# Kernel tuning notes

Measured on AMD Instinct MI355X. Metric: run time of the kernel, lower is better.

## Reference

```python
import jax, jax.numpy as jnp
import numpy as np

# Layered type graph: L layers of M nodes; layer 0 = basic types, layers >=1 reference earlier layers only.
L, M, D, P, S = 64, 2048, 128, 4, 2
NB = 11  # number of Kotlin basic types (kotlin.Any ... kotlin.Unit)
N = L * M


def setup_inputs() -> dict:
    key = jax.random.key(0)
    ks = jax.random.split(key, 8)
    rng = np.random.default_rng(0)
    basic_names = jnp.asarray(rng.integers(0, NB, size=(M,)), dtype=jnp.int32)
    # properties / superTypes point strictly to earlier layers (valid topological DAG)
    prop_ids = np.zeros((L, M, P), dtype=np.int32)
    super_ids = np.zeros((L, M, S), dtype=np.int32)
    for l in range(1, L):
        prop_ids[l] = rng.integers(0, l * M, size=(M, P))
        super_ids[l] = rng.integers(0, l * M, size=(M, S))
    prop_ids = jnp.asarray(prop_ids)
    super_ids = jnp.asarray(super_ids)
    sc = 0.05
    return {
        "basic_names": basic_names,
        "prop_ids": prop_ids,
        "super_ids": super_ids,
        "basic_table": jax.random.normal(ks[0], (NB, D), jnp.float32) * sc,
        "W_m": jax.random.normal(ks[1], (D, 4 * D), jnp.float32) * sc,
        "U_m": jax.random.normal(ks[2], (D, 4 * D), jnp.float32) * sc,
        "b_m": jnp.zeros((4 * D,), jnp.float32),
        "W_s": jax.random.normal(ks[3], (D, 4 * D), jnp.float32) * sc,
        "U_s": jax.random.normal(ks[4], (D, 4 * D), jnp.float32) * sc,
        "b_s": jnp.zeros((4 * D,), jnp.float32),
        "empty_members": jax.random.normal(ks[5], (D,), jnp.float32) * sc,
    }


def _lstm_last(seq, W, U, b):
    # seq: [T, B, D]; keras LSTM (tanh / sigmoid, gate order i,f,g,o); returns last hidden [B, D]
    T, B, Dh = seq.shape
    h = jnp.zeros((B, Dh), seq.dtype)
    c = jnp.zeros((B, Dh), seq.dtype)
    for t in range(T):  # T is a small static constant (P+1 or S+1)
        z = seq[t] @ W + h @ U + b  # [B, 4D]
        i, f, g, o = jnp.split(z, 4, axis=-1)
        c = jax.nn.sigmoid(f) * c + jax.nn.sigmoid(i) * jnp.tanh(g)
        h = jax.nn.sigmoid(o) * jnp.tanh(c)
    return h


def reference(basic_names, prop_ids, super_ids, basic_table, W_m, U_m, b_m, W_s, U_s, b_s, empty_members):
    emb = jnp.zeros((N, D), basic_table.dtype)
    emb = emb.at[:M].set(basic_table[basic_names])  # layer 0: basic type embedding lookup

    def step(emb, xs):
        l, pid, sid = xs  # pid:[M,P] sid:[M,S], all indices < l*M (already computed)
        prop_e = jnp.swapaxes(emb[pid], 0, 1)  # [P, M, D] irregular gather
        seq_m = jnp.concatenate([jnp.broadcast_to(empty_members, (1, M, D)), prop_e], axis=0)  # [P+1, M, D]
        h_m = _lstm_last(seq_m, W_m, U_m, b_m)  # embed_members
        sup_e = jnp.swapaxes(emb[sid], 0, 1)  # [S, M, D]
        seq_s = jnp.concatenate([sup_e, h_m[None]], axis=0)  # [S+1, M, D]
        h_s = _lstm_last(seq_s, W_s, U_s, b_s)  # embed_super_types
        emb = jax.lax.dynamic_update_slice(emb, h_s, (l * M, 0))
        return emb, None

    ls = jnp.arange(1, L, dtype=jnp.int32)
    emb, _ = jax.lax.scan(step, emb, (ls, prop_ids[1:], super_ids[1:]))
    return emb  # [N, D] == tf.convert_to_tensor(class_embeddings)
```

## Files before the change

kernel.cpp:

```cpp
#include <hip/hip_runtime.h>

typedef unsigned short u16;
typedef short s16x8 __attribute__((ext_vector_type(8)));
typedef float f32x4 __attribute__((ext_vector_type(4)));

#define LAYERS   64
#define M_NODES  2048
#define DIM      128
#define FD       512
#define CHUNK    16
#define NBLK     128
#define TPB      512
#define XPAD     136

__device__ __forceinline__ u16 f2bf(float f) {
    union { float f; unsigned int i; } v; v.f = f;
    unsigned int r = (v.i + 0x7FFFu + ((v.i >> 16) & 1u)) >> 16;
    return (u16)r;
}
__device__ __forceinline__ float sigm(float x) {
    return __builtin_amdgcn_rcpf(1.0f + __builtin_exp2f(-1.44269504f * x));
}
__device__ __forceinline__ float tanh_f(float x) {
    float ax = __builtin_fabsf(x);
    float t  = __builtin_exp2f(-2.88539008f * ax);
    float r  = (1.0f - t) * __builtin_amdgcn_rcpf(1.0f + t);
    return __builtin_copysignf(r, x);
}

__global__ void l0_kernel(const int* __restrict__ names, const float* __restrict__ table,
                          float* __restrict__ emb) {
    int v = blockIdx.x * blockDim.x + threadIdx.x;
    if (v >= M_NODES * (DIM / 4)) return;
    int row = v >> 5, c = v & 31;
    const float4* src = (const float4*)(table + (size_t)names[row] * DIM);
    ((float4*)(emb + (size_t)row * DIM))[c] = src[c];
}

__global__ void repack_kernel(const float* __restrict__ Wm, const float* __restrict__ Um,
                              const float* __restrict__ Ws, const float* __restrict__ Us,
                              u16* __restrict__ packed) {
    int t = blockIdx.x * blockDim.x + threadIdx.x;
    if (t >= 4 * 4 * 32 * 64) return;
    int lane = t & 63, ntg = (t >> 6) & 31, kc = (t >> 11) & 3, mat = t >> 13;
    const float* B = (mat == 0) ? Wm : (mat == 1) ? Um : (mat == 2) ? Ws : Us;
    int q = lane >> 4, nl = lane & 15;
    int kb = kc * 32 + q * 8;
    int n  = ntg * 16 + nl;
    u16* dst = packed + ((((size_t)mat * 4 + kc) * 32 + ntg) * 64 + lane) * 8;
    #pragma unroll
    for (int j = 0; j < 8; j++) dst[j] = f2bf(B[(size_t)(kb + j) * FD + n]);
}

template <bool PACKED>
__global__ __launch_bounds__(TPB, 2) void layer_kernel(
    float* __restrict__ emb, const int* __restrict__ prop_ids, const int* __restrict__ super_ids,
    const float* __restrict__ Wm, const float* __restrict__ Um, const float* __restrict__ bm,
    const float* __restrict__ Ws, const float* __restrict__ Us, const float* __restrict__ bs,
    const float* __restrict__ empty, const u16* __restrict__ packed, int l) {

    __shared__ __align__(16) u16  xs[6][CHUNK][XPAD];
    __shared__ __align__(16) u16  hbuf[2][CHUNK][XPAD];
    __shared__ __align__(16) u16  empty_s[XPAD];

    const int tid  = threadIdx.x;
    const int b    = blockIdx.x;
    const int g0   = b * CHUNK;
    const size_t row0 = (size_t)l * M_NODES + g0;

    const int wv   = tid >> 6;
    const int lane = tid & 63;
    const int q    = lane >> 4, nl = lane & 15;
    const int d    = wv * 16 + nl;

    if (tid < 384) {
        int quarter = tid & 3;
        int r    = tid >> 2;
        int slot = r >> 4;
        int node = r & 15;
        size_t idx;
        if (slot < 4) idx = (size_t)prop_ids [((size_t)l * M_NODES + g0 + node) * 4 + slot];
        else          idx = (size_t)super_ids[((size_t)l * M_NODES + g0 + node) * 2 + (slot - 4)];
        const float4* src = (const float4*)(emb + idx * DIM);
        u16* dst = &xs[slot][node][0];
        int e0 = quarter * 32;
        #pragma unroll
        for (int j = 0; j < 8; j++) {
            float4 v = src[(e0 >> 2) + j];
            int o = e0 + j * 4;
            dst[o] = f2bf(v.x); dst[o + 1] = f2bf(v.y);
            dst[o + 2] = f2bf(v.z); dst[o + 3] = f2bf(v.w);
        }
    } else if (tid < 384 + 128) {
        int dd = tid - 384;
        empty_s[dd] = f2bf(empty[dd]);
    }
    __syncthreads();

    auto load_bfrag_packed = [&](int mat, int kc, int g) -> s16x8 {
        return *(const s16x8*)(packed + ((((size_t)mat * 4 + kc) * 32 + (g * 8 + wv)) * 64 + lane) * 8);
    };
    auto load_bfrag_direct = [&](const float* B, int kc, int g) -> s16x8 {
        int kb = kc * 32 + q * 8;
        int n  = g * 128 + d;
        s16x8 f;
        #pragma unroll
        for (int j = 0; j < 8; j++) f[j] = (short)f2bf(B[(size_t)(kb + j) * FD + n]);
        return f;
    };
    auto load_afrag = [&](const u16* X , int kc) -> s16x8 {
        return *(const s16x8*)(X + (size_t)nl * XPAD + kc * 32 + q * 8);
    };

    auto run_phase = [&](const float* Wg, const float* Ug, const float* bias,
                         int matW, int matU, int nsteps, const int* slots,
                         bool write_hm, bool write_out) {
        s16x8 wf[4][4], uf[4][4];
        #pragma unroll
        for (int kc = 0; kc < 4; kc++) {
            #pragma unroll
            for (int g = 0; g < 4; g++) {
                if (PACKED) { wf[kc][g] = load_bfrag_packed(matW, kc, g);
                              uf[kc][g] = load_bfrag_packed(matU, kc, g); }
                else        { wf[kc][g] = load_bfrag_direct(Wg, kc, g);
                              uf[kc][g] = load_bfrag_direct(Ug, kc, g); }
            }
        }
        float bz[4];
        #pragma unroll
        for (int g = 0; g < 4; g++) bz[g] = bias[g * 128 + d];
        float cc[4] = {0.f, 0.f, 0.f, 0.f};

        #pragma unroll 1
        for (int t = 0; t < nsteps; t++) {
            int s = slots[t];
            f32x4 acc[4];
            #pragma unroll
            for (int g = 0; g < 4; g++) acc[g] = (f32x4){0.f, 0.f, 0.f, 0.f};
            #pragma unroll
            for (int kc = 0; kc < 4; kc++) {
                s16x8 a = (s < 0) ? *(const s16x8*)(&empty_s[kc * 32 + q * 8])
                                  : load_afrag(&xs[s][0][0], kc);
                #pragma unroll
                for (int g = 0; g < 4; g++)
                    acc[g] = __builtin_amdgcn_mfma_f32_16x16x32_bf16(a, wf[kc][g], acc[g], 0, 0, 0);
            }
            if (t > 0) {
                __syncthreads();
                const u16* hb = &hbuf[(t - 1) & 1][0][0];
                #pragma unroll
                for (int kc = 0; kc < 4; kc++) {
                    s16x8 a = load_afrag(hb, kc);
                    #pragma unroll
                    for (int g = 0; g < 4; g++)
                        acc[g] = __builtin_amdgcn_mfma_f32_16x16x32_bf16(a, uf[kc][g], acc[g], 0, 0, 0);
                }
            }
            bool last = (t == nsteps - 1);
            #pragma unroll
            for (int r2 = 0; r2 < 4; r2++) {
                int m = q * 4 + r2;
                float zi = acc[0][r2] + bz[0];
                float zf = acc[1][r2] + bz[1];
                float zg = acc[2][r2] + bz[2];
                float zo = acc[3][r2] + bz[3];
                float c  = sigm(zf) * cc[r2] + sigm(zi) * tanh_f(zg);
                cc[r2] = c;
                float h  = sigm(zo) * tanh_f(c);
                if (!last)          hbuf[t & 1][m][d] = f2bf(h);
                else if (write_hm)  xs[0][m][d] = f2bf(h);
                else if (write_out) emb[(row0 + m) * DIM + d] = h;
            }
        }
    };

    {
        const int slots_m[5] = {-1, 0, 1, 2, 3};
        run_phase(Wm, Um, bm, 0, 1, 5, slots_m, true, false);
    }
    {
        const int slots_s[3] = {4, 5, 0};
        run_phase(Ws, Us, bs, 2, 3, 3, slots_s, false, true);
    }
}

extern "C" void kernel_launch(void* const* d_in, const int* in_sizes, int n_in,
                              void* d_out, int out_size, void* d_ws, size_t ws_size,
                              hipStream_t stream) {
    const int*   names = (const int*)d_in[0];
    const int*   pids  = (const int*)d_in[1];
    const int*   sids  = (const int*)d_in[2];
    const float* table = (const float*)d_in[3];
    const float* Wm    = (const float*)d_in[4];
    const float* Um    = (const float*)d_in[5];
    const float* bm    = (const float*)d_in[6];
    const float* Ws    = (const float*)d_in[7];
    const float* Us    = (const float*)d_in[8];
    const float* bs    = (const float*)d_in[9];
    const float* empt  = (const float*)d_in[10];
    float* emb  = (float*)d_out;
    u16* packed = (u16*)d_ws;

    l0_kernel<<<256, 256, 0, stream>>>(names, table, emb);

    const size_t packed_bytes = (size_t)4 * 4 * 32 * 64 * 8 * sizeof(u16);
    if (ws_size >= packed_bytes) {
        repack_kernel<<<128, 256, 0, stream>>>(Wm, Um, Ws, Us, packed);
        for (int l = 1; l < LAYERS; l++)
            layer_kernel<true><<<NBLK, TPB, 0, stream>>>(emb, pids, sids, Wm, Um, bm,
                                                         Ws, Us, bs, empt, packed, l);
    } else {
        for (int l = 1; l < LAYERS; l++)
            layer_kernel<false><<<NBLK, TPB, 0, stream>>>(emb, pids, sids, Wm, Um, bm,
                                                          Ws, Us, bs, empt, packed, l);
    }
}
```

Baseline: 1.269 ms.

## Replace per-layer launches with persistent cooperative kernel and global atomic barrier

```diff
diff --git a/kernel.cpp b/kernel.cpp
--- a/kernel.cpp
+++ b/kernel.cpp
@@ -52,85 +52,176 @@
     for (int j = 0; j < 8; j++) dst[j] = f2bf(B[(size_t)(kb + j) * FD + n]);
 }
 
-template <bool PACKED>
-__global__ __launch_bounds__(TPB, 2) void layer_kernel(
+__global__ void init_bar(int* bar) { if (threadIdx.x < 2) bar[threadIdx.x] = 0; }
+
+__device__ __forceinline__ s16x8 load_bfrag(const u16* __restrict__ packed,
+                                            int mat, int kc, int ntile, int lane) {
+    return *(const s16x8*)(packed + ((((size_t)mat * 4 + kc) * 32 + ntile) * 64 + lane) * 8);
+}
+
+template<int NSTEPS>
+__device__ __forceinline__ void lstm_phase(
+    const u16* __restrict__ packed, const int matW, const int matU,
+    const float* __restrict__ bz , const int* slots,
+    u16 (*xs)[CHUNK][XPAD], u16 (*hbuf)[CHUNK][XPAD], const u16* empty_s,
+    float* __restrict__ out ,
+    const int wv, const int lane)
+{
+    const int q = lane >> 4, nl = lane & 15;
+    const int d = wv * 16 + nl;
+    s16x8 wf[4][4], uf[4][4];
+    #pragma unroll
+    for (int kc = 0; kc < 4; kc++)
+        #pragma unroll
+        for (int g = 0; g < 4; g++) {
+            wf[kc][g] = load_bfrag(packed, matW, kc, g * 8 + wv, lane);
+            uf[kc][g] = load_bfrag(packed, matU, kc, g * 8 + wv, lane);
+        }
+    float cc[4] = {0.f, 0.f, 0.f, 0.f};
+    #pragma unroll
+    for (int t = 0; t < NSTEPS; t++) {
+        const int s = slots[t];
+        f32x4 acc[4];
+        #pragma unroll
+        for (int g = 0; g < 4; g++) acc[g] = (f32x4){0.f, 0.f, 0.f, 0.f};
+        #pragma unroll
+        for (int kc = 0; kc < 4; kc++) {
+            s16x8 a = (s < 0) ? *(const s16x8*)(empty_s + kc * 32 + q * 8)
+                              : *(const s16x8*)(&xs[s][nl][kc * 32 + q * 8]);
+            #pragma unroll
+            for (int g = 0; g < 4; g++)
+                acc[g] = __builtin_amdgcn_mfma_f32_16x16x32_bf16(a, wf[kc][g], acc[g], 0, 0, 0);
+        }
+        if (t > 0) {
+            __syncthreads();
+            #pragma unroll
+            for (int kc = 0; kc < 4; kc++) {
+                s16x8 a = *(const s16x8*)(&hbuf[(t - 1) & 1][nl][kc * 32 + q * 8]);
+                #pragma unroll
+                for (int g = 0; g < 4; g++)
+                    acc[g] = __builtin_amdgcn_mfma_f32_16x16x32_bf16(a, uf[kc][g], acc[g], 0, 0, 0);
+            }
+        }
+        const bool last = (t == NSTEPS - 1);
+        #pragma unroll
+        for (int r2 = 0; r2 < 4; r2++) {
+            int m = q * 4 + r2;
+            float zi = acc[0][r2] + bz[0];
+            float zf = acc[1][r2] + bz[1];
+            float zg = acc[2][r2] + bz[2];
+            float zo = acc[3][r2] + bz[3];
+            float c  = sigm(zf) * cc[r2] + sigm(zi) * tanh_f(zg);
+            cc[r2] = c;
+            float h  = sigm(zo) * tanh_f(c);
+            if (!last)            hbuf[t & 1][m][d] = f2bf(h);
+            else if (out == nullptr) xs[0][m][d] = f2bf(h);
+            else                  out[(size_t)m * DIM + d] = h;
+        }
+    }
+}
+
+__global__ __launch_bounds__(TPB, 2) void persist_kernel(
+    float* __restrict__ emb, const int* __restrict__ prop_ids, const int* __restrict__ super_ids,
+    const float* __restrict__ bm, const float* __restrict__ bs,
+    const float* __restrict__ empty, const u16* __restrict__ packed, int* bar) {
+
+    __shared__ __align__(16) u16  xs[6][CHUNK][XPAD];
+    __shared__ __align__(16) u16  hbuf[2][CHUNK][XPAD];
+    __shared__ __align__(16) u16  empty_s[XPAD];
+
+    const int tid  = threadIdx.x;
+    const int g0   = blockIdx.x * CHUNK;
+    const int wv   = tid >> 6;
+    const int lane = tid & 63;
+    const int d    = wv * 16 + (lane & 15);
+
+    if (tid < DIM) empty_s[tid] = f2bf(empty[tid]);
+    float bzm[4], bzs[4];
+    #pragma unroll
+    for (int g = 0; g < 4; g++) { bzm[g] = bm[g * 128 + d]; bzs[g] = bs[g * 128 + d]; }
+
+    const int c32  = tid & 31;
+    const int node = tid >> 5;
+
+    #pragma unroll 1
+    for (int l = 1; l < LAYERS; l++) {
+        #pragma unroll
+        for (int k = 0; k < 6; k++) {
+            int idx = (k < 4) ? prop_ids [((size_t)l * M_NODES + g0 + node) * 4 + k]
+                              : super_ids[((size_t)l * M_NODES + g0 + node) * 2 + (k - 4)];
+            float4 v = ((const float4*)(emb + (size_t)idx * DIM))[c32];
+            u16* dst = &xs[k][node][c32 * 4];
+            dst[0] = f2bf(v.x); dst[1] = f2bf(v.y); dst[2] = f2bf(v.z); dst[3] = f2bf(v.w);
+        }
+        __syncthreads();
+
+        const int slots_m[5] = {-1, 0, 1, 2, 3};
+        lstm_phase<5>(packed, 0, 1, bzm, slots_m, xs, hbuf, empty_s, nullptr, wv, lane);
+        const int slots_s[3] = {4, 5, 0};
+        lstm_phase<3>(packed, 2, 3, bzs, slots_s, xs, hbuf, empty_s,
+                      emb + ((size_t)l * M_NODES + g0) * DIM, wv, lane);
+
+        if (l < LAYERS - 1) {
+            __syncthreads();
+            if (tid == 0) {
+                __builtin_amdgcn_fence(__ATOMIC_RELEASE, "agent");
+                __hip_atomic_fetch_add(bar, 1, __ATOMIC_RELAXED, __HIP_MEMORY_SCOPE_AGENT);
+                const int target = l * NBLK;
+                while (__hip_atomic_load(bar, __ATOMIC_RELAXED, __HIP_MEMORY_SCOPE_AGENT) < target)
+                    __builtin_amdgcn_s_sleep(2);
+                __builtin_amdgcn_fence(__ATOMIC_ACQUIRE, "agent");
+            }
+            __syncthreads();
+        }
+    }
+}
+
+__global__ __launch_bounds__(TPB, 2) void layer_fallback(
     float* __restrict__ emb, const int* __restrict__ prop_ids, const int* __restrict__ super_ids,
     const float* __restrict__ Wm, const float* __restrict__ Um, const float* __restrict__ bm,
     const float* __restrict__ Ws, const float* __restrict__ Us, const float* __restrict__ bs,
-    const float* __restrict__ empty, const u16* __restrict__ packed, int l) {
+    const float* __restrict__ empty, int l) {
 
     __shared__ __align__(16) u16  xs[6][CHUNK][XPAD];
     __shared__ __align__(16) u16  hbuf[2][CHUNK][XPAD];
     __shared__ __align__(16) u16  empty_s[XPAD];
 
     const int tid  = threadIdx.x;
-    const int b    = blockIdx.x;
-    const int g0   = b * CHUNK;
-    const size_t row0 = (size_t)l * M_NODES + g0;
-
-    const int wv   = tid >> 6;
-    const int lane = tid & 63;
+    const int g0   = blockIdx.x * CHUNK;
+    const int wv   = tid >> 6, lane = tid & 63;
     const int q    = lane >> 4, nl = lane & 15;
     const int d    = wv * 16 + nl;
-
-    if (tid < 384) {
-        int quarter = tid & 3;
-        int r    = tid >> 2;
-        int slot = r >> 4;
-        int node = r & 15;
-        size_t idx;
-        if (slot < 4) idx = (size_t)prop_ids [((size_t)l * M_NODES + g0 + node) * 4 + slot];
-        else          idx = (size_t)super_ids[((size_t)l * M_NODES + g0 + node) * 2 + (slot - 4)];
-        const float4* src = (const float4*)(emb + idx * DIM);
-        u16* dst = &xs[slot][node][0];
-        int e0 = quarter * 32;
-        #pragma unroll
-        for (int j = 0; j < 8; j++) {
-            float4 v = src[(e0 >> 2) + j];
-            int o = e0 + j * 4;
-            dst[o] = f2bf(v.x); dst[o + 1] = f2bf(v.y);
-            dst[o + 2] = f2bf(v.z); dst[o + 3] = f2bf(v.w);
-        }
-    } else if (tid < 384 + 128) {
-        int dd = tid - 384;
-        empty_s[dd] = f2bf(empty[dd]);
+    const int c32  = tid & 31, node = tid >> 5;
+
+    if (tid < DIM) empty_s[tid] = f2bf(empty[tid]);
+    #pragma unroll
+    for (int k = 0; k < 6; k++) {
+        int idx = (k < 4) ? prop_ids [((size_t)l * M_NODES + g0 + node) * 4 + k]
+                          : super_ids[((size_t)l * M_NODES + g0 + node) * 2 + (k - 4)];
+        float4 v = ((const float4*)(emb + (size_t)idx * DIM))[c32];
+        u16* dst = &xs[k][node][c32 * 4];
+        dst[0] = f2bf(v.x); dst[1] = f2bf(v.y); dst[2] = f2bf(v.z); dst[3] = f2bf(v.w);
     }
     __syncthreads();
 
-    auto load_bfrag_packed = [&](int mat, int kc, int g) -> s16x8 {
-        return *(const s16x8*)(packed + ((((size_t)mat * 4 + kc) * 32 + (g * 8 + wv)) * 64 + lane) * 8);
-    };
-    auto load_bfrag_direct = [&](const float* B, int kc, int g) -> s16x8 {
-        int kb = kc * 32 + q * 8;
-        int n  = g * 128 + d;
+    auto direct = [&](const float* B, int kc, int g) -> s16x8 {
+        int kb = kc * 32 + q * 8, n = g * 128 + d;
         s16x8 f;
         #pragma unroll
         for (int j = 0; j < 8; j++) f[j] = (short)f2bf(B[(size_t)(kb + j) * FD + n]);
         return f;
     };
-    auto load_afrag = [&](const u16* X , int kc) -> s16x8 {
-        return *(const s16x8*)(X + (size_t)nl * XPAD + kc * 32 + q * 8);
-    };
-
-    auto run_phase = [&](const float* Wg, const float* Ug, const float* bias,
-                         int matW, int matU, int nsteps, const int* slots,
-                         bool write_hm, bool write_out) {
+    auto run = [&](const float* W, const float* U, const float* bias,
+                   int nsteps, const int* slots, float* out) {
         s16x8 wf[4][4], uf[4][4];
         #pragma unroll
-        for (int kc = 0; kc < 4; kc++) {
-            #pragma unroll
-            for (int g = 0; g < 4; g++) {
-                if (PACKED) { wf[kc][g] = load_bfrag_packed(matW, kc, g);
-                              uf[kc][g] = load_bfrag_packed(matU, kc, g); }
-                else        { wf[kc][g] = load_bfrag_direct(Wg, kc, g);
-                              uf[kc][g] = load_bfrag_direct(Ug, kc, g); }
-            }
-        }
+        for (int kc = 0; kc < 4; kc++)
+            #pragma unroll
+            for (int g = 0; g < 4; g++) { wf[kc][g] = direct(W, kc, g); uf[kc][g] = direct(U, kc, g); }
         float bz[4];
         #pragma unroll
         for (int g = 0; g < 4; g++) bz[g] = bias[g * 128 + d];
         float cc[4] = {0.f, 0.f, 0.f, 0.f};
-
         #pragma unroll 1
         for (int t = 0; t < nsteps; t++) {
             int s = slots[t];
@@ -139,18 +230,17 @@
             for (int g = 0; g < 4; g++) acc[g] = (f32x4){0.f, 0.f, 0.f, 0.f};
             #pragma unroll
             for (int kc = 0; kc < 4; kc++) {
-                s16x8 a = (s < 0) ? *(const s16x8*)(&empty_s[kc * 32 + q * 8])
-                                  : load_afrag(&xs[s][0][0], kc);
+                s16x8 a = (s < 0) ? *(const s16x8*)(empty_s + kc * 32 + q * 8)
+                                  : *(const s16x8*)(&xs[s][nl][kc * 32 + q * 8]);
                 #pragma unroll
                 for (int g = 0; g < 4; g++)
                     acc[g] = __builtin_amdgcn_mfma_f32_16x16x32_bf16(a, wf[kc][g], acc[g], 0, 0, 0);
             }
             if (t > 0) {
                 __syncthreads();
-                const u16* hb = &hbuf[(t - 1) & 1][0][0];
                 #pragma unroll
                 for (int kc = 0; kc < 4; kc++) {
-                    s16x8 a = load_afrag(hb, kc);
+                    s16x8 a = *(const s16x8*)(&hbuf[(t - 1) & 1][nl][kc * 32 + q * 8]);
                     #pragma unroll
                     for (int g = 0; g < 4; g++)
                         acc[g] = __builtin_amdgcn_mfma_f32_16x16x32_bf16(a, uf[kc][g], acc[g], 0, 0, 0);
@@ -167,21 +257,16 @@
                 float c  = sigm(zf) * cc[r2] + sigm(zi) * tanh_f(zg);
                 cc[r2] = c;
                 float h  = sigm(zo) * tanh_f(c);
-                if (!last)          hbuf[t & 1][m][d] = f2bf(h);
-                else if (write_hm)  xs[0][m][d] = f2bf(h);
-                else if (write_out) emb[(row0 + m) * DIM + d] = h;
+                if (!last)               hbuf[t & 1][m][d] = f2bf(h);
+                else if (out == nullptr) xs[0][m][d] = f2bf(h);
+                else                     out[(size_t)m * DIM + d] = h;
             }
         }
     };
-
-    {
-        const int slots_m[5] = {-1, 0, 1, 2, 3};
-        run_phase(Wm, Um, bm, 0, 1, 5, slots_m, true, false);
-    }
-    {
-        const int slots_s[3] = {4, 5, 0};
-        run_phase(Ws, Us, bs, 2, 3, 3, slots_s, false, true);
-    }
+    const int slots_m[5] = {-1, 0, 1, 2, 3};
+    run(Wm, Um, bm, 5, slots_m, nullptr);
+    const int slots_s[3] = {4, 5, 0};
+    run(Ws, Us, bs, 3, slots_s, emb + ((size_t)l * M_NODES + g0) * DIM);
 }
 
 extern "C" void kernel_launch(void* const* d_in, const int* in_sizes, int n_in,
@@ -199,19 +284,23 @@
     const float* bs    = (const float*)d_in[9];
     const float* empt  = (const float*)d_in[10];
     float* emb  = (float*)d_out;
+
+    const size_t packed_bytes = (size_t)4 * 4 * 32 * 64 * 8 * sizeof(u16);
     u16* packed = (u16*)d_ws;
+    int* bar    = (int*)((char*)d_ws + packed_bytes);
 
     l0_kernel<<<256, 256, 0, stream>>>(names, table, emb);
 
-    const size_t packed_bytes = (size_t)4 * 4 * 32 * 64 * 8 * sizeof(u16);
-    if (ws_size >= packed_bytes) {
+    if (ws_size >= packed_bytes + 256) {
         repack_kernel<<<128, 256, 0, stream>>>(Wm, Um, Ws, Us, packed);
-        for (int l = 1; l < LAYERS; l++)
-            layer_kernel<true><<<NBLK, TPB, 0, stream>>>(emb, pids, sids, Wm, Um, bm,
-                                                         Ws, Us, bs, empt, packed, l);
+        init_bar<<<1, 64, 0, stream>>>(bar);
+        void* args[] = {(void*)&emb, (void*)&pids, (void*)&sids, (void*)&bm, (void*)&bs,
+                        (void*)&empt, (void*)&packed, (void*)&bar};
+        hipLaunchCooperativeKernel((const void*)persist_kernel, dim3(NBLK), dim3(TPB),
+                                   args, 0, stream);
     } else {
         for (int l = 1; l < LAYERS; l++)
-            layer_kernel<false><<<NBLK, TPB, 0, stream>>>(emb, pids, sids, Wm, Um, bm,
-                                                          Ws, Us, bs, empt, packed, l);
+            layer_fallback<<<NBLK, TPB, 0, stream>>>(emb, pids, sids, Wm, Um, bm,
+                                                     Ws, Us, bs, empt, l);
     }
 }
```

New measurement: 1.933 ms. 1.52x slower.
